# Kernel optimization log

Hardware: AMD Instinct MI355X
Metric: run time of the kernel (lower is better)

## Reference

```python
import jax, jax.numpy as jnp
import numpy as np

EMBED_DIM = 768
NUM_HEAD = 12
HEAD_DIM = 64
SCALE = 1.0 / np.sqrt(HEAD_DIM)


def setup_inputs() -> dict:
    key = jax.random.key(0)
    k1, k2, k3, k4 = jax.random.split(key, 4)
    B, T = 2, 2048
    x = jax.random.normal(k1, (B, T, EMBED_DIM), dtype=jnp.float32)
    # nn.Linear(embed_dim, 3*embed_dim, bias=True): weight [3E, E], bias [3E]
    w_qkv = jax.random.normal(k2, (3 * EMBED_DIM, EMBED_DIM), dtype=jnp.float32) * (1.0 / np.sqrt(EMBED_DIM))
    b_qkv = jax.random.normal(k3, (3 * EMBED_DIM,), dtype=jnp.float32) * 0.02
    # nn.Linear(embed_dim, embed_dim, bias=False): weight [E, E]
    w_final = jax.random.normal(k4, (EMBED_DIM, EMBED_DIM), dtype=jnp.float32) * (1.0 / np.sqrt(EMBED_DIM))
    return {"x": x, "w_qkv": w_qkv, "b_qkv": b_qkv, "w_final": w_final}


def reference(x, w_qkv, b_qkv, w_final):
    B, T, E = x.shape
    # qkv projection: x @ W^T + b  -> [B, T, 3E]
    qkv = jnp.einsum('bte,fe->btf', x, w_qkv) + b_qkv
    q, k, v = jnp.split(qkv, 3, axis=-1)

    def heads(t):  # [B, T, E] -> [B, H, T, D]
        return t.reshape(B, T, NUM_HEAD, HEAD_DIM).transpose(0, 2, 1, 3)

    q, k, v = heads(q), heads(k), heads(v)
    # scores [B, H, T, T]
    scores = jnp.einsum('bhtd,bhsd->bhts', q, k) * SCALE
    causal = jnp.tril(jnp.ones((T, T), dtype=bool))
    scores = jnp.where(causal, scores, -jnp.inf)
    attn = jax.nn.softmax(scores, axis=-1)  # dropout off (eval mode)
    out = jnp.einsum('bhts,bhsd->bhtd', attn, v)  # [B, H, T, D]
    out = out.transpose(0, 2, 1, 3).reshape(B, T, NUM_HEAD * HEAD_DIM)
    return jnp.einsum('bte,fe->btf', out, w_final)
```

## Files before the change

kernel.cpp:

```cpp
#include <hip/hip_runtime.h>
#include <cstdint>

typedef _Float16 f16x8 __attribute__((ext_vector_type(8)));
typedef _Float16 f16x4 __attribute__((ext_vector_type(4)));
typedef float    f32x4 __attribute__((ext_vector_type(4)));

static constexpr int TB = 2;
static constexpr int TT = 2048;
static constexpr int TE = 768;
static constexpr int TH = 12;
static constexpr int TD = 64;
static constexpr int TM = TB * TT;
static constexpr int TK = TE;
static constexpr int NQKV = 3 * TE;

#define SCALE_LOG2E 0.18033688011112042f

__device__ __forceinline__ void gload16(const void* g, void* lds) {
  __builtin_amdgcn_global_load_lds(
      (__attribute__((address_space(1))) void*)(uintptr_t)g,
      (__attribute__((address_space(3))) void*)(uint32_t)(uintptr_t)lds, 16, 0, 0);
}

__global__ void cvt3(const float* __restrict__ x, const float* __restrict__ wq,
                     const float* __restrict__ wf, _Float16* __restrict__ xh,
                     _Float16* __restrict__ wqh, _Float16* __restrict__ wfh) {
  const int NX = TM * TK / 4, NW = NQKV * TK / 4;
  int i = blockIdx.x * 256 + threadIdx.x;
  if (i < NX) {
    float4 v = ((const float4*)x)[i];
    f16x4 o = {(_Float16)v.x, (_Float16)v.y, (_Float16)v.z, (_Float16)v.w};
    *(f16x4*)&xh[(size_t)i * 4] = o;
  } else {
    const float4* src; _Float16* dst; int j;
    if (i < NX + NW) { src = (const float4*)wq; dst = wqh; j = i - NX; }
    else             { src = (const float4*)wf; dst = wfh; j = i - NX - NW; }
    float4 v = src[j];
    f16x4 o = {(_Float16)v.x, (_Float16)v.y, (_Float16)v.z, (_Float16)v.w};
    const int flat = j * 4;
    const int n = flat / TK, k = flat % TK;
    const size_t idx = ((size_t)(n >> 4) * 24 + (k >> 5)) * 512 +
                       ((k >> 3) & 3) * 128 + (n & 15) * 8 + (k & 7);
    *(f16x4*)&dst[idx] = o;
  }
}

template <int EPI, int NXT>
__global__ __launch_bounds__(512)
void gemm_nt(const _Float16* __restrict__ A, const _Float16* __restrict__ Bw,
             const float* __restrict__ bias,
             _Float16* __restrict__ qb, _Float16* __restrict__ kb,
             _Float16* __restrict__ vtb, float* __restrict__ outp) {
  __shared__ _Float16 As[2][128 * 64];
  const int tid = threadIdx.x;
  const int w = tid >> 6, lane = tid & 63;
  const int lr = lane & 15, lk = lane >> 4;

  const int id = blockIdx.x;
  const int xcd = id & 7, j = id >> 3;
  const int m0 = (xcd * 4 + j / NXT) * 128;
  const int n0 = (j % NXT) * 128;
  const int wr = w >> 2, wc = w & 3;

  f32x4 acc[4][2] = {};
  const char* Ab = (const char*)(A + (size_t)m0 * TK);
  const char* WB = (const char*)Bw;
  const int nb = (n0 >> 4) + wc * 2;
  constexpr int NS = TK / 64;

  auto loadB = [&](int ks, f16x8 (&bf)[2][2]) {
#pragma unroll
    for (int ni = 0; ni < 2; ++ni)
#pragma unroll
      for (int kc = 0; kc < 2; ++kc)
        bf[ni][kc] = *(const f16x8*)(WB +
                                     ((size_t)(nb + ni) * 24 + ks * 2 + kc) * 1024 +
                                     lane * 16);
  };
  auto stageA = [&](int ks, int buf) {
#pragma unroll
    for (int c = 0; c < 2; ++c) {
      int g = w * 2 + c;
      int o = g * 1024 + lane * 16;
      int row = o >> 7, ch = (o >> 4) & 7;
      gload16(Ab + (size_t)row * (TK * 2) + ks * 128 + ((ch ^ (row & 7)) << 4),
              (char*)As[buf] + g * 1024);
    }
  };
  auto step = [&](f16x8 (&bc)[2][2], f16x8 (&bn)[2][2], int buf, int ks) {
    if (ks + 1 < NS) {
      loadB(ks + 1, bn);
      stageA(ks + 1, buf ^ 1);
      asm volatile("s_waitcnt vmcnt(6)" ::: "memory");
    } else {
      asm volatile("s_waitcnt vmcnt(0)" ::: "memory");
    }
    __builtin_amdgcn_s_barrier();
#pragma unroll
    for (int kc = 0; kc < 2; ++kc) {
      f16x8 af[4];
#pragma unroll
      for (int mi = 0; mi < 4; ++mi) {
        int row = wr * 64 + mi * 16 + lr;
        af[mi] =
            *(const f16x8*)&As[buf][row * 64 + (((kc * 4 + lk) ^ (row & 7)) << 3)];
      }
#pragma unroll
      for (int mi = 0; mi < 4; ++mi)
#pragma unroll
        for (int ni = 0; ni < 2; ++ni)
          acc[mi][ni] = __builtin_amdgcn_mfma_f32_16x16x32_f16(af[mi], bc[ni][kc],
                                                               acc[mi][ni], 0, 0, 0);
    }
    __builtin_amdgcn_s_barrier();
  };

  f16x8 bA[2][2], bB[2][2];
  loadB(0, bA);
  stageA(0, 0);
  for (int kss = 0; kss < NS; kss += 2) {
    step(bA, bB, 0, kss);
    step(bB, bA, 1, kss + 1);
  }

#pragma unroll
  for (int mi = 0; mi < 4; ++mi) {
#pragma unroll
    for (int ni = 0; ni < 2; ++ni) {
      const int col = n0 + wc * 32 + ni * 16 + lr;
#pragma unroll
      for (int r = 0; r < 4; ++r) {
        const int row = m0 + wr * 64 + mi * 16 + lk * 4 + r;
        float v = acc[mi][ni][r];
        if (EPI == 0) {
          v += bias[col];
          const int which = (col >= 2 * TE) ? 2 : (col >= TE ? 1 : 0);
          const int e = col - which * TE;
          const int h = e >> 6, d = e & 63;
          const int b = row >> 11, t = row & (TT - 1);
          const size_t hb = (size_t)(b * TH + h);
          if (which == 0) {
            qb[(hb * TT + t) * TD + d] = (_Float16)(v * SCALE_LOG2E);
          } else if (which == 1) {
            kb[((((hb * 128 + (t >> 4)) * 8 + (d >> 3)) * 16 + (t & 15)) * 8) +
               (d & 7)] = (_Float16)v;
          } else {
            const int kc = (t >> 5) & 1, hi = (t >> 4) & 1;
            const int lkv = (t >> 2) & 3, m = t & 3;
            vtb[((((((hb * 32 + (t >> 6)) * 4 + (d >> 4)) * 2 + kc) * 4 + lkv) *
                      16 +
                  (d & 15)) *
                 8) +
                (hi * 4 + m)] = (_Float16)v;
          }
        } else {
          outp[(size_t)row * TE + col] = v;
        }
      }
    }
  }
}

__global__ __launch_bounds__(128)
void attn_kernel(const _Float16* __restrict__ qbuf, const _Float16* __restrict__ kbuf,
                 const _Float16* __restrict__ vtbuf, _Float16* __restrict__ ob) {
  const int tid = threadIdx.x, w = tid >> 6, lane = tid & 63;
  const int lr = lane & 15, lk = lane >> 4;

  const int id = blockIdx.x;
  const int bh = id % 24;
  const int qt = 31 - id / 24;
  const int t0 = qt * 64;
  const int nt = qt + 1, ntm1 = qt;
  const int q0 = t0 + w * 32;

  const _Float16* q = qbuf + (size_t)bh * (TT * TD);
  const char* kbase =
      (const char*)(kbuf + (size_t)bh * (TT * TD)) + lk * 256 + lr * 16;
  const char* vbase =
      (const char*)(vtbuf + (size_t)bh * (TT * TD)) + lk * 256 + lr * 16;

  f16x8 qf0[2], qf1[2];
#pragma unroll
  for (int kc = 0; kc < 2; ++kc) {
    qf0[kc] = *(const f16x8*)&q[(size_t)(q0 + lr) * TD + kc * 32 + lk * 8];
    qf1[kc] = *(const f16x8*)&q[(size_t)(q0 + 16 + lr) * TD + kc * 32 + lk * 8];
  }

  f32x4 of0[4] = {}, of1[4] = {};
  float mr0 = -1e30f, ls0 = 0.f;
  float mr1 = -1e30f, ls1 = 0.f;

  f16x8 kfA[2][4], kfB[2][4], vf[2][4];

#pragma unroll
  for (int kc = 0; kc < 2; ++kc)
#pragma unroll
    for (int ni = 0; ni < 4; ++ni)
      kfA[kc][ni] = *(const f16x8*)(kbase + ni * 2048 + kc * 1024);
  {
    const char* k1 = kbase + (size_t)(nt > 1 ? 1 : 0) * 8192;
#pragma unroll
    for (int kc = 0; kc < 2; ++kc)
#pragma unroll
      for (int ni = 0; ni < 4; ++ni)
        kfB[kc][ni] = *(const f16x8*)(k1 + ni * 2048 + kc * 1024);
  }

  auto sm_pv = [&](f32x4 (&sa)[4], float& mr, float& ls, f32x4 (&of_)[4],
                   int qb_, int s0, bool dia) {
    if (dia) {
#pragma unroll
      for (int ni = 0; ni < 4; ++ni)
#pragma unroll
        for (int r = 0; r < 4; ++r)
          if (s0 + ni * 16 + lk * 4 + r > qb_ + lr) sa[ni][r] = -1e30f;
    }
    float mx;
    {
      float a0 = fmaxf(fmaxf(sa[0][0], sa[0][1]), fmaxf(sa[0][2], sa[0][3]));
      float a1 = fmaxf(fmaxf(sa[1][0], sa[1][1]), fmaxf(sa[1][2], sa[1][3]));
      float a2 = fmaxf(fmaxf(sa[2][0], sa[2][1]), fmaxf(sa[2][2], sa[2][3]));
      float a3 = fmaxf(fmaxf(sa[3][0], sa[3][1]), fmaxf(sa[3][2], sa[3][3]));
      mx = fmaxf(fmaxf(a0, a1), fmaxf(a2, a3));
      mx = fmaxf(mx, __shfl_xor(mx, 16));
      mx = fmaxf(mx, __shfl_xor(mx, 32));
    }
    if (__any(mx > mr + 8.0f)) {
      float mn = fmaxf(mr, mx);
      float al = __builtin_amdgcn_exp2f(mr - mn);
      mr = mn;
      ls *= al;
      float al4[4];
#pragma unroll
      for (int r = 0; r < 4; ++r) al4[r] = __shfl(al, lk * 4 + r);
#pragma unroll
      for (int nd = 0; nd < 4; ++nd)
#pragma unroll
        for (int r = 0; r < 4; ++r) of_[nd][r] *= al4[r];
    }
    f16x8 pa[2];
    float rs;
    {
      float rn[4];
#pragma unroll
      for (int ni = 0; ni < 4; ++ni) {
        float p0 = __builtin_amdgcn_exp2f(sa[ni][0] - mr);
        float p1 = __builtin_amdgcn_exp2f(sa[ni][1] - mr);
        float p2 = __builtin_amdgcn_exp2f(sa[ni][2] - mr);
        float p3 = __builtin_amdgcn_exp2f(sa[ni][3] - mr);
        rn[ni] = (p0 + p1) + (p2 + p3);
        pa[ni >> 1][(ni & 1) * 4 + 0] = (_Float16)p0;
        pa[ni >> 1][(ni & 1) * 4 + 1] = (_Float16)p1;
        pa[ni >> 1][(ni & 1) * 4 + 2] = (_Float16)p2;
        pa[ni >> 1][(ni & 1) * 4 + 3] = (_Float16)p3;
      }
      rs = (rn[0] + rn[1]) + (rn[2] + rn[3]);
      rs += __shfl_xor(rs, 16);
      rs += __shfl_xor(rs, 32);
    }
    ls += rs;
    __builtin_amdgcn_s_setprio(1);
#pragma unroll
    for (int kc = 0; kc < 2; ++kc)
#pragma unroll
      for (int nd = 0; nd < 4; ++nd)
        of_[nd] =
            __builtin_amdgcn_mfma_f32_16x16x32_f16(pa[kc], vf[kc][nd], of_[nd], 0, 0, 0);
    __builtin_amdgcn_s_setprio(0);
  };

  auto phase = [&](f16x8 (&kf)[2][4], int st) {
    const char* vt = vbase + (size_t)st * 8192;
#pragma unroll
    for (int kc = 0; kc < 2; ++kc)
#pragma unroll
      for (int nd = 0; nd < 4; ++nd)
        vf[kc][nd] = *(const f16x8*)(vt + nd * 2048 + kc * 1024);

    f32x4 sa0[4] = {}, sa1[4] = {};
    __builtin_amdgcn_s_setprio(1);
#pragma unroll
    for (int kc = 0; kc < 2; ++kc)
#pragma unroll
      for (int ni = 0; ni < 4; ++ni)
        sa0[ni] =
            __builtin_amdgcn_mfma_f32_16x16x32_f16(kf[kc][ni], qf0[kc], sa0[ni], 0, 0, 0);
#pragma unroll
    for (int kc = 0; kc < 2; ++kc)
#pragma unroll
      for (int ni = 0; ni < 4; ++ni)
        sa1[ni] =
            __builtin_amdgcn_mfma_f32_16x16x32_f16(kf[kc][ni], qf1[kc], sa1[ni], 0, 0, 0);
    __builtin_amdgcn_s_setprio(0);

    {
      const int stp = (st + 2 <= ntm1) ? st + 2 : ntm1;
      const char* kt = kbase + (size_t)stp * 8192;
#pragma unroll
      for (int kc = 0; kc < 2; ++kc)
#pragma unroll
        for (int ni = 0; ni < 4; ++ni)
          kf[kc][ni] = *(const f16x8*)(kt + ni * 2048 + kc * 1024);
    }

    const int s0 = st * 64;
    sm_pv(sa0, mr0, ls0, of0, q0, s0, s0 + 63 > q0);
    sm_pv(sa1, mr1, ls1, of1, q0 + 16, s0, s0 + 63 > q0 + 16);
  };

  int st = 0;
  while (st + 1 < nt) {
    phase(kfA, st);
    phase(kfB, st + 1);
    st += 2;
  }
  if (st < nt) phase(kfA, st);

  const int b = bh / TH, h = bh - b * TH;
  {
    float linv[4];
#pragma unroll
    for (int r = 0; r < 4; ++r) linv[r] = __shfl(ls0, lk * 4 + r);
#pragma unroll
    for (int nd = 0; nd < 4; ++nd)
#pragma unroll
      for (int r = 0; r < 4; ++r) {
        int tg = q0 + lk * 4 + r;
        int d = nd * 16 + lr;
        ob[(size_t)(b * TT + tg) * TE + h * TD + d] = (_Float16)(of0[nd][r] / linv[r]);
      }
  }
  {
    float linv[4];
#pragma unroll
    for (int r = 0; r < 4; ++r) linv[r] = __shfl(ls1, lk * 4 + r);
#pragma unroll
    for (int nd = 0; nd < 4; ++nd)
#pragma unroll
      for (int r = 0; r < 4; ++r) {
        int tg = q0 + 16 + lk * 4 + r;
        int d = nd * 16 + lr;
        ob[(size_t)(b * TT + tg) * TE + h * TD + d] = (_Float16)(of1[nd][r] / linv[r]);
      }
  }
}

extern "C" void kernel_launch(void* const* d_in, const int* in_sizes, int n_in,
                              void* d_out, int out_size, void* d_ws, size_t ws_size,
                              hipStream_t stream) {
  const float* x    = (const float*)d_in[0];
  const float* wqkv = (const float*)d_in[1];
  const float* bqkv = (const float*)d_in[2];
  const float* wfin = (const float*)d_in[3];
  float* out = (float*)d_out;

  _Float16* xh  = (_Float16*)d_ws;
  _Float16* wqh = xh + (size_t)TM * TK;
  _Float16* wfh = wqh + (size_t)NQKV * TK;
  _Float16* qb  = wfh + (size_t)TE * TE;
  _Float16* kb  = qb + (size_t)TM * TE;
  _Float16* vtb = kb + (size_t)TM * TE;
  _Float16* ob  = vtb + (size_t)TM * TE;

  cvt3<<<5376, 256, 0, stream>>>(x, wqkv, wfin, xh, wqh, wfh);
  gemm_nt<0, NQKV / 128><<<(NQKV / 128) * (TM / 128), 512, 0, stream>>>(
      xh, wqh, bqkv, qb, kb, vtb, nullptr);
  attn_kernel<<<dim3(TT / 64 * TB * TH), 128, 0, stream>>>(qb, kb, vtb, ob);
  gemm_nt<1, TE / 128><<<(TE / 128) * (TM / 128), 512, 0, stream>>>(
      ob, wfh, nullptr, nullptr, nullptr, nullptr, out);
}
```

Measured before the change: 93.81 us.

## Split attention KV loop across two waves per query group with LDS merge

```diff
diff --git a/kernel.cpp b/kernel.cpp
--- a/kernel.cpp
+++ b/kernel.cpp
@@ -161,18 +161,20 @@
   }
 }
 
-__global__ __launch_bounds__(128)
+__global__ __launch_bounds__(256)
 void attn_kernel(const _Float16* __restrict__ qbuf, const _Float16* __restrict__ kbuf,
                  const _Float16* __restrict__ vtbuf, _Float16* __restrict__ ob) {
+  __shared__ float Om[2][32][65];
+  __shared__ float Mm[2][32], Ll[2][32];
   const int tid = threadIdx.x, w = tid >> 6, lane = tid & 63;
   const int lr = lane & 15, lk = lane >> 4;
+  const int h = w >> 1, p = w & 1;
 
   const int id = blockIdx.x;
   const int bh = id % 24;
   const int qt = 31 - id / 24;
   const int t0 = qt * 64;
-  const int nt = qt + 1, ntm1 = qt;
-  const int q0 = t0 + w * 32;
+  const int q0 = t0 + h * 32;
 
   const _Float16* q = qbuf + (size_t)bh * (TT * TD);
   const char* kbase =
@@ -191,20 +193,21 @@
   float mr0 = -1e30f, ls0 = 0.f;
   float mr1 = -1e30f, ls1 = 0.f;
 
+  const int slast = (p <= qt) ? (qt - ((qt - p) & 1)) : 0;
+
   f16x8 kfA[2][4], kfB[2][4], vf[2][4];
-
-#pragma unroll
-  for (int kc = 0; kc < 2; ++kc)
-#pragma unroll
-    for (int ni = 0; ni < 4; ++ni)
-      kfA[kc][ni] = *(const f16x8*)(kbase + ni * 2048 + kc * 1024);
   {
-    const char* k1 = kbase + (size_t)(nt > 1 ? 1 : 0) * 8192;
-#pragma unroll
-    for (int kc = 0; kc < 2; ++kc)
-#pragma unroll
-      for (int ni = 0; ni < 4; ++ni)
-        kfB[kc][ni] = *(const f16x8*)(k1 + ni * 2048 + kc * 1024);
+    const int tA = (p <= qt) ? p : 0;
+    const int tBt = (p + 2 <= qt) ? p + 2 : tA;
+    const char* ka = kbase + (size_t)tA * 8192;
+    const char* kb2 = kbase + (size_t)tBt * 8192;
+#pragma unroll
+    for (int kc = 0; kc < 2; ++kc)
+#pragma unroll
+      for (int ni = 0; ni < 4; ++ni) {
+        kfA[kc][ni] = *(const f16x8*)(ka + ni * 2048 + kc * 1024);
+        kfB[kc][ni] = *(const f16x8*)(kb2 + ni * 2048 + kc * 1024);
+      }
   }
 
   auto sm_pv = [&](f32x4 (&sa)[4], float& mr, float& ls, f32x4 (&of_)[4],
@@ -295,7 +298,7 @@
     __builtin_amdgcn_s_setprio(0);
 
     {
-      const int stp = (st + 2 <= ntm1) ? st + 2 : ntm1;
+      const int stp = (st + 4 <= qt) ? st + 4 : slast;
       const char* kt = kbase + (size_t)stp * 8192;
 #pragma unroll
       for (int kc = 0; kc < 2; ++kc)
@@ -305,44 +308,60 @@
     }
 
     const int s0 = st * 64;
-    sm_pv(sa0, mr0, ls0, of0, q0, s0, s0 + 63 > q0);
-    sm_pv(sa1, mr1, ls1, of1, q0 + 16, s0, s0 + 63 > q0 + 16);
-  };
-
-  int st = 0;
-  while (st + 1 < nt) {
+    const bool dia = (st == qt);
+    sm_pv(sa0, mr0, ls0, of0, q0, s0, dia);
+    sm_pv(sa1, mr1, ls1, of1, q0 + 16, s0, dia);
+  };
+
+  int st = p;
+  while (st + 2 <= qt) {
     phase(kfA, st);
-    phase(kfB, st + 1);
-    st += 2;
-  }
-  if (st < nt) phase(kfA, st);
-
-  const int b = bh / TH, h = bh - b * TH;
-  {
-    float linv[4];
-#pragma unroll
-    for (int r = 0; r < 4; ++r) linv[r] = __shfl(ls0, lk * 4 + r);
+    phase(kfB, st + 2);
+    st += 4;
+  }
+  if (st <= qt) phase(kfA, st);
+
+  if (p == 1) {
 #pragma unroll
     for (int nd = 0; nd < 4; ++nd)
 #pragma unroll
       for (int r = 0; r < 4; ++r) {
-        int tg = q0 + lk * 4 + r;
-        int d = nd * 16 + lr;
-        ob[(size_t)(b * TT + tg) * TE + h * TD + d] = (_Float16)(of0[nd][r] / linv[r]);
-      }
-  }
-  {
-    float linv[4];
-#pragma unroll
-    for (int r = 0; r < 4; ++r) linv[r] = __shfl(ls1, lk * 4 + r);
-#pragma unroll
-    for (int nd = 0; nd < 4; ++nd)
+        Om[h][lk * 4 + r][nd * 16 + lr] = of0[nd][r];
+        Om[h][16 + lk * 4 + r][nd * 16 + lr] = of1[nd][r];
+      }
+    if (lk == 0) {
+      Mm[h][lr] = mr0;
+      Ll[h][lr] = ls0;
+      Mm[h][16 + lr] = mr1;
+      Ll[h][16 + lr] = ls1;
+    }
+  }
+  __syncthreads();
+  if (p == 0) {
+    const int b = bh / TH, hh = bh - b * TH;
+#pragma unroll
+    for (int sub = 0; sub < 2; ++sub) {
+      f32x4* ofp = sub ? of1 : of0;
+      float mrs = sub ? mr1 : mr0, lss = sub ? ls1 : ls0;
 #pragma unroll
       for (int r = 0; r < 4; ++r) {
-        int tg = q0 + 16 + lk * 4 + r;
-        int d = nd * 16 + lr;
-        ob[(size_t)(b * TT + tg) * TE + h * TD + d] = (_Float16)(of1[nd][r] / linv[r]);
-      }
+        const int qq = sub * 16 + lk * 4 + r;
+        float m0 = __shfl(mrs, lk * 4 + r);
+        float l0 = __shfl(lss, lk * 4 + r);
+        float m1 = Mm[h][qq], l1 = Ll[h][qq];
+        float ms = fmaxf(m0, m1);
+        float a0 = __builtin_amdgcn_exp2f(m0 - ms);
+        float a1 = __builtin_amdgcn_exp2f(m1 - ms);
+        float rden = 1.0f / (l0 * a0 + l1 * a1);
+        float c0 = a0 * rden, c1 = a1 * rden;
+#pragma unroll
+        for (int nd = 0; nd < 4; ++nd) {
+          const int d = nd * 16 + lr;
+          float val = ofp[nd][r] * c0 + Om[h][qq][d] * c1;
+          ob[(size_t)(b * TT + q0 + qq) * TE + hh * TD + d] = (_Float16)val;
+        }
+      }
+    }
   }
 }
 
@@ -366,7 +385,7 @@
   cvt3<<<5376, 256, 0, stream>>>(x, wqkv, wfin, xh, wqh, wfh);
   gemm_nt<0, NQKV / 128><<<(NQKV / 128) * (TM / 128), 512, 0, stream>>>(
       xh, wqh, bqkv, qb, kb, vtb, nullptr);
-  attn_kernel<<<dim3(TT / 64 * TB * TH), 128, 0, stream>>>(qb, kb, vtb, ob);
+  attn_kernel<<<dim3(TT / 64 * TB * TH), 256, 0, stream>>>(qb, kb, vtb, ob);
   gemm_nt<1, TE / 128><<<(TE / 128) * (TM / 128), 512, 0, stream>>>(
       ob, wfh, nullptr, nullptr, nullptr, nullptr, out);
 }
```

New measurement: 94.52 us. No clear change (+0.8%).

## Use 4-wave attention blocks with atomic work-stealing over query tiles

Applied to the files above, without the earlier changes.

```diff
diff --git a/kernel.cpp b/kernel.cpp
--- a/kernel.cpp
+++ b/kernel.cpp
@@ -13,6 +13,7 @@
 static constexpr int TM = TB * TT;
 static constexpr int TK = TE;
 static constexpr int NQKV = 3 * TE;
+static constexpr int NUNITS = 24 * 32;
 
 #define SCALE_LOG2E 0.18033688011112042f
 
@@ -161,188 +162,172 @@
   }
 }
 
-__global__ __launch_bounds__(128)
+__global__ __launch_bounds__(256)
 void attn_kernel(const _Float16* __restrict__ qbuf, const _Float16* __restrict__ kbuf,
-                 const _Float16* __restrict__ vtbuf, _Float16* __restrict__ ob) {
+                 const _Float16* __restrict__ vtbuf, _Float16* __restrict__ ob,
+                 int* __restrict__ ctr) {
+  __shared__ int s_unit;
   const int tid = threadIdx.x, w = tid >> 6, lane = tid & 63;
   const int lr = lane & 15, lk = lane >> 4;
 
-  const int id = blockIdx.x;
-  const int bh = id % 24;
-  const int qt = 31 - id / 24;
-  const int t0 = qt * 64;
-  const int nt = qt + 1, ntm1 = qt;
-  const int q0 = t0 + w * 32;
-
-  const _Float16* q = qbuf + (size_t)bh * (TT * TD);
-  const char* kbase =
-      (const char*)(kbuf + (size_t)bh * (TT * TD)) + lk * 256 + lr * 16;
-  const char* vbase =
-      (const char*)(vtbuf + (size_t)bh * (TT * TD)) + lk * 256 + lr * 16;
-
-  f16x8 qf0[2], qf1[2];
-#pragma unroll
-  for (int kc = 0; kc < 2; ++kc) {
-    qf0[kc] = *(const f16x8*)&q[(size_t)(q0 + lr) * TD + kc * 32 + lk * 8];
-    qf1[kc] = *(const f16x8*)&q[(size_t)(q0 + 16 + lr) * TD + kc * 32 + lk * 8];
-  }
-
-  f32x4 of0[4] = {}, of1[4] = {};
-  float mr0 = -1e30f, ls0 = 0.f;
-  float mr1 = -1e30f, ls1 = 0.f;
-
-  f16x8 kfA[2][4], kfB[2][4], vf[2][4];
-
-#pragma unroll
-  for (int kc = 0; kc < 2; ++kc)
-#pragma unroll
-    for (int ni = 0; ni < 4; ++ni)
-      kfA[kc][ni] = *(const f16x8*)(kbase + ni * 2048 + kc * 1024);
-  {
-    const char* k1 = kbase + (size_t)(nt > 1 ? 1 : 0) * 8192;
+  for (;;) {
+    __syncthreads();
+    if (tid == 0) s_unit = atomicAdd(ctr, 1);
+    __syncthreads();
+    const int u = s_unit;
+    if (u >= NUNITS) break;
+
+    const int bh = u % 24;
+    const int qt = 31 - u / 24;
+    const int t0 = qt * 64;
+    const int nt = qt + 1, ntm1 = qt;
+
+    const _Float16* q = qbuf + (size_t)bh * (TT * TD);
+    const char* kbase =
+        (const char*)(kbuf + (size_t)bh * (TT * TD)) + lk * 256 + lr * 16;
+    const char* vbase =
+        (const char*)(vtbuf + (size_t)bh * (TT * TD)) + lk * 256 + lr * 16;
+
+    f16x8 qf[2];
 #pragma unroll
     for (int kc = 0; kc < 2; ++kc)
+      qf[kc] = *(const f16x8*)&q[(size_t)(t0 + w * 16 + lr) * TD + kc * 32 + lk * 8];
+
+    f32x4 of[4] = {};
+    float mrun = -1e30f, lrun = 0.f;
+
+    f16x8 kfA[2][4], kfB[2][4], vf[2][4];
+
+#pragma unroll
+    for (int kc = 0; kc < 2; ++kc)
 #pragma unroll
       for (int ni = 0; ni < 4; ++ni)
-        kfB[kc][ni] = *(const f16x8*)(k1 + ni * 2048 + kc * 1024);
-  }
-
-  auto sm_pv = [&](f32x4 (&sa)[4], float& mr, float& ls, f32x4 (&of_)[4],
-                   int qb_, int s0, bool dia) {
-    if (dia) {
-#pragma unroll
-      for (int ni = 0; ni < 4; ++ni)
-#pragma unroll
-        for (int r = 0; r < 4; ++r)
-          if (s0 + ni * 16 + lk * 4 + r > qb_ + lr) sa[ni][r] = -1e30f;
-    }
-    float mx;
+        kfA[kc][ni] = *(const f16x8*)(kbase + ni * 2048 + kc * 1024);
     {
-      float a0 = fmaxf(fmaxf(sa[0][0], sa[0][1]), fmaxf(sa[0][2], sa[0][3]));
-      float a1 = fmaxf(fmaxf(sa[1][0], sa[1][1]), fmaxf(sa[1][2], sa[1][3]));
-      float a2 = fmaxf(fmaxf(sa[2][0], sa[2][1]), fmaxf(sa[2][2], sa[2][3]));
-      float a3 = fmaxf(fmaxf(sa[3][0], sa[3][1]), fmaxf(sa[3][2], sa[3][3]));
-      mx = fmaxf(fmaxf(a0, a1), fmaxf(a2, a3));
-      mx = fmaxf(mx, __shfl_xor(mx, 16));
-      mx = fmaxf(mx, __shfl_xor(mx, 32));
-    }
-    if (__any(mx > mr + 8.0f)) {
-      float mn = fmaxf(mr, mx);
-      float al = __builtin_amdgcn_exp2f(mr - mn);
-      mr = mn;
-      ls *= al;
-      float al4[4];
-#pragma unroll
-      for (int r = 0; r < 4; ++r) al4[r] = __shfl(al, lk * 4 + r);
-#pragma unroll
-      for (int nd = 0; nd < 4; ++nd)
-#pragma unroll
-        for (int r = 0; r < 4; ++r) of_[nd][r] *= al4[r];
-    }
-    f16x8 pa[2];
-    float rs;
-    {
-      float rn[4];
-#pragma unroll
-      for (int ni = 0; ni < 4; ++ni) {
-        float p0 = __builtin_amdgcn_exp2f(sa[ni][0] - mr);
-        float p1 = __builtin_amdgcn_exp2f(sa[ni][1] - mr);
-        float p2 = __builtin_amdgcn_exp2f(sa[ni][2] - mr);
-        float p3 = __builtin_amdgcn_exp2f(sa[ni][3] - mr);
-        rn[ni] = (p0 + p1) + (p2 + p3);
-        pa[ni >> 1][(ni & 1) * 4 + 0] = (_Float16)p0;
-        pa[ni >> 1][(ni & 1) * 4 + 1] = (_Float16)p1;
-        pa[ni >> 1][(ni & 1) * 4 + 2] = (_Float16)p2;
-        pa[ni >> 1][(ni & 1) * 4 + 3] = (_Float16)p3;
-      }
-      rs = (rn[0] + rn[1]) + (rn[2] + rn[3]);
-      rs += __shfl_xor(rs, 16);
-      rs += __shfl_xor(rs, 32);
-    }
-    ls += rs;
-    __builtin_amdgcn_s_setprio(1);
-#pragma unroll
-    for (int kc = 0; kc < 2; ++kc)
-#pragma unroll
-      for (int nd = 0; nd < 4; ++nd)
-        of_[nd] =
-            __builtin_amdgcn_mfma_f32_16x16x32_f16(pa[kc], vf[kc][nd], of_[nd], 0, 0, 0);
-    __builtin_amdgcn_s_setprio(0);
-  };
-
-  auto phase = [&](f16x8 (&kf)[2][4], int st) {
-    const char* vt = vbase + (size_t)st * 8192;
-#pragma unroll
-    for (int kc = 0; kc < 2; ++kc)
-#pragma unroll
-      for (int nd = 0; nd < 4; ++nd)
-        vf[kc][nd] = *(const f16x8*)(vt + nd * 2048 + kc * 1024);
-
-    f32x4 sa0[4] = {}, sa1[4] = {};
-    __builtin_amdgcn_s_setprio(1);
-#pragma unroll
-    for (int kc = 0; kc < 2; ++kc)
-#pragma unroll
-      for (int ni = 0; ni < 4; ++ni)
-        sa0[ni] =
-            __builtin_amdgcn_mfma_f32_16x16x32_f16(kf[kc][ni], qf0[kc], sa0[ni], 0, 0, 0);
-#pragma unroll
-    for (int kc = 0; kc < 2; ++kc)
-#pragma unroll
-      for (int ni = 0; ni < 4; ++ni)
-        sa1[ni] =
-            __builtin_amdgcn_mfma_f32_16x16x32_f16(kf[kc][ni], qf1[kc], sa1[ni], 0, 0, 0);
-    __builtin_amdgcn_s_setprio(0);
-
-    {
-      const int stp = (st + 2 <= ntm1) ? st + 2 : ntm1;
-      const char* kt = kbase + (size_t)stp * 8192;
+      const char* k1 = kbase + (size_t)(nt > 1 ? 1 : 0) * 8192;
 #pragma unroll
       for (int kc = 0; kc < 2; ++kc)
 #pragma unroll
         for (int ni = 0; ni < 4; ++ni)
-          kf[kc][ni] = *(const f16x8*)(kt + ni * 2048 + kc * 1024);
-    }
-
-    const int s0 = st * 64;
-    sm_pv(sa0, mr0, ls0, of0, q0, s0, s0 + 63 > q0);
-    sm_pv(sa1, mr1, ls1, of1, q0 + 16, s0, s0 + 63 > q0 + 16);
-  };
-
-  int st = 0;
-  while (st + 1 < nt) {
-    phase(kfA, st);
-    phase(kfB, st + 1);
-    st += 2;
-  }
-  if (st < nt) phase(kfA, st);
-
-  const int b = bh / TH, h = bh - b * TH;
-  {
+          kfB[kc][ni] = *(const f16x8*)(k1 + ni * 2048 + kc * 1024);
+    }
+
+    auto phase = [&](f16x8 (&kf)[2][4], int st) {
+      const char* vt = vbase + (size_t)st * 8192;
+#pragma unroll
+      for (int kc = 0; kc < 2; ++kc)
+#pragma unroll
+        for (int nd = 0; nd < 4; ++nd)
+          vf[kc][nd] = *(const f16x8*)(vt + nd * 2048 + kc * 1024);
+
+      f32x4 sa[4] = {};
+      __builtin_amdgcn_s_setprio(1);
+#pragma unroll
+      for (int kc = 0; kc < 2; ++kc)
+#pragma unroll
+        for (int ni = 0; ni < 4; ++ni)
+          sa[ni] = __builtin_amdgcn_mfma_f32_16x16x32_f16(kf[kc][ni], qf[kc],
+                                                          sa[ni], 0, 0, 0);
+      __builtin_amdgcn_s_setprio(0);
+
+      {
+        const int stp = (st + 2 <= ntm1) ? st + 2 : ntm1;
+        const char* kt = kbase + (size_t)stp * 8192;
+#pragma unroll
+        for (int kc = 0; kc < 2; ++kc)
+#pragma unroll
+          for (int ni = 0; ni < 4; ++ni)
+            kf[kc][ni] = *(const f16x8*)(kt + ni * 2048 + kc * 1024);
+      }
+
+      if (st == ntm1) {
+        const int s0 = st * 64;
+#pragma unroll
+        for (int ni = 0; ni < 4; ++ni)
+#pragma unroll
+          for (int r = 0; r < 4; ++r)
+            if (s0 + ni * 16 + lk * 4 + r > t0 + w * 16 + lr) sa[ni][r] = -1e30f;
+      }
+
+      float mx;
+      {
+        float a0 = fmaxf(fmaxf(sa[0][0], sa[0][1]), fmaxf(sa[0][2], sa[0][3]));
+        float a1 = fmaxf(fmaxf(sa[1][0], sa[1][1]), fmaxf(sa[1][2], sa[1][3]));
+        float a2 = fmaxf(fmaxf(sa[2][0], sa[2][1]), fmaxf(sa[2][2], sa[2][3]));
+        float a3 = fmaxf(fmaxf(sa[3][0], sa[3][1]), fmaxf(sa[3][2], sa[3][3]));
+        mx = fmaxf(fmaxf(a0, a1), fmaxf(a2, a3));
+        mx = fmaxf(mx, __shfl_xor(mx, 16));
+        mx = fmaxf(mx, __shfl_xor(mx, 32));
+      }
+
+      if (__any(mx > mrun + 8.0f)) {
+        float mn = fmaxf(mrun, mx);
+        float al = __builtin_amdgcn_exp2f(mrun - mn);
+        mrun = mn;
+        lrun *= al;
+        float al4[4];
+#pragma unroll
+        for (int r = 0; r < 4; ++r) al4[r] = __shfl(al, lk * 4 + r);
+#pragma unroll
+        for (int nd = 0; nd < 4; ++nd)
+#pragma unroll
+          for (int r = 0; r < 4; ++r) of[nd][r] *= al4[r];
+      }
+
+      f16x8 pa[2];
+      float rs;
+      {
+        float rn[4];
+#pragma unroll
+        for (int ni = 0; ni < 4; ++ni) {
+          float p0 = __builtin_amdgcn_exp2f(sa[ni][0] - mrun);
+          float p1 = __builtin_amdgcn_exp2f(sa[ni][1] - mrun);
+          float p2 = __builtin_amdgcn_exp2f(sa[ni][2] - mrun);
+          float p3 = __builtin_amdgcn_exp2f(sa[ni][3] - mrun);
+          rn[ni] = (p0 + p1) + (p2 + p3);
+          pa[ni >> 1][(ni & 1) * 4 + 0] = (_Float16)p0;
+          pa[ni >> 1][(ni & 1) * 4 + 1] = (_Float16)p1;
+          pa[ni >> 1][(ni & 1) * 4 + 2] = (_Float16)p2;
+          pa[ni >> 1][(ni & 1) * 4 + 3] = (_Float16)p3;
+        }
+        rs = (rn[0] + rn[1]) + (rn[2] + rn[3]);
+        rs += __shfl_xor(rs, 16);
+        rs += __shfl_xor(rs, 32);
+      }
+      lrun += rs;
+
+      __builtin_amdgcn_s_setprio(1);
+#pragma unroll
+      for (int kc = 0; kc < 2; ++kc)
+#pragma unroll
+        for (int nd = 0; nd < 4; ++nd)
+          of[nd] = __builtin_amdgcn_mfma_f32_16x16x32_f16(pa[kc], vf[kc][nd],
+                                                          of[nd], 0, 0, 0);
+      __builtin_amdgcn_s_setprio(0);
+    };
+
+    int st = 0;
+    while (st + 1 < nt) {
+      phase(kfA, st);
+      phase(kfB, st + 1);
+      st += 2;
+    }
+    if (st < nt) phase(kfA, st);
+
     float linv[4];
 #pragma unroll
-    for (int r = 0; r < 4; ++r) linv[r] = __shfl(ls0, lk * 4 + r);
-#pragma unroll
-    for (int nd = 0; nd < 4; ++nd)
+    for (int r = 0; r < 4; ++r) linv[r] = __shfl(lrun, lk * 4 + r);
+    const int b = bh / TH, h = bh - b * TH;
+#pragma unroll
+    for (int nd = 0; nd < 4; ++nd) {
 #pragma unroll
       for (int r = 0; r < 4; ++r) {
-        int tg = q0 + lk * 4 + r;
+        int tg = t0 + w * 16 + lk * 4 + r;
         int d = nd * 16 + lr;
-        ob[(size_t)(b * TT + tg) * TE + h * TD + d] = (_Float16)(of0[nd][r] / linv[r]);
-      }
-  }
-  {
-    float linv[4];
-#pragma unroll
-    for (int r = 0; r < 4; ++r) linv[r] = __shfl(ls1, lk * 4 + r);
-#pragma unroll
-    for (int nd = 0; nd < 4; ++nd)
-#pragma unroll
-      for (int r = 0; r < 4; ++r) {
-        int tg = q0 + 16 + lk * 4 + r;
-        int d = nd * 16 + lr;
-        ob[(size_t)(b * TT + tg) * TE + h * TD + d] = (_Float16)(of1[nd][r] / linv[r]);
-      }
+        ob[(size_t)(b * TT + tg) * TE + h * TD + d] =
+            (_Float16)(of[nd][r] / linv[r]);
+      }
+    }
   }
 }
 
@@ -362,11 +347,13 @@
   _Float16* kb  = qb + (size_t)TM * TE;
   _Float16* vtb = kb + (size_t)TM * TE;
   _Float16* ob  = vtb + (size_t)TM * TE;
-
+  int* ctr = (int*)(ob + (size_t)TM * TE);
+
+  hipMemsetAsync(ctr, 0, 4, stream);
   cvt3<<<5376, 256, 0, stream>>>(x, wqkv, wfin, xh, wqh, wfh);
   gemm_nt<0, NQKV / 128><<<(NQKV / 128) * (TM / 128), 512, 0, stream>>>(
       xh, wqh, bqkv, qb, kb, vtb, nullptr);
-  attn_kernel<<<dim3(TT / 64 * TB * TH), 128, 0, stream>>>(qb, kb, vtb, ob);
+  attn_kernel<<<dim3(TT / 64 * TB * TH), 256, 0, stream>>>(qb, kb, vtb, ob, ctr);
   gemm_nt<1, TE / 128><<<(TE / 128) * (TM / 128), 512, 0, stream>>>(
       ob, wfh, nullptr, nullptr, nullptr, nullptr, out);
 }
```

Result: slower. 102.6 us (+9.4%).
